# Optimization experiments

Measured on AMD Instinct MI355X. Metric: run time of the kernel, lower is better.

## Reference

```python
import jax, jax.numpy as jnp
import numpy as np

B, C, H, W = 512, 2048, 8, 8   # batch, backbone channels, feature-map HxW (cfg.output_hm_shape)
J = 30                          # smpl.pos_joint_num
CF = 512                        # conv output channels
EPS = 1e-5                      # BatchNorm eps


def setup_inputs() -> dict:
    key = jax.random.key(0)
    ks = jax.random.split(key, 10)
    D = J * (CF + 3)  # 15450
    return {
        "img_feat": jax.random.normal(ks[0], (B, C, H, W), jnp.float32),
        # joint coords in heatmap pixel space [0, W-1] (x, y, z)
        "joint_coord_img": jax.random.uniform(ks[1], (B, J, 3), jnp.float32) * (W - 1),
        "conv_w": jax.random.normal(ks[2], (CF, C), jnp.float32) * 0.02,
        "conv_b": jnp.zeros((CF,), jnp.float32),
        "bn_gamma": jnp.ones((CF,), jnp.float32),
        "bn_beta": jnp.zeros((CF,), jnp.float32),
        "bn_mean": jnp.zeros((CF,), jnp.float32),
        "bn_var": jnp.ones((CF,), jnp.float32),
        "root_w": jax.random.normal(ks[3], (6, D), jnp.float32) * 0.01,
        "root_b": jnp.zeros((6,), jnp.float32),
        "pose_w": jax.random.normal(ks[4], (126, D), jnp.float32) * 0.01,
        "pose_b": jnp.zeros((126,), jnp.float32),
        "shape_w": jax.random.normal(ks[5], (10, C), jnp.float32) * 0.01,
        "shape_b": jnp.zeros((10,), jnp.float32),
        "cam_w": jax.random.normal(ks[6], (3, C), jnp.float32) * 0.01,
        "cam_b": jnp.zeros((3,), jnp.float32),
    }


def _bilinear_sample(feat, xy):
    """Batched bilinear sample == F.grid_sample(align_corners=True, padding='zeros')
    with grid built directly from pixel coords in [0, W-1].
    feat: (B, Cf, H, W), xy: (B, J, 2) pixel coords -> (B, J, Cf)."""
    x, y = xy[..., 0], xy[..., 1]
    x0f, y0f = jnp.floor(x), jnp.floor(y)
    wx1, wy1 = x - x0f, y - y0f
    wx0, wy0 = 1.0 - wx1, 1.0 - wy1
    x0, y0 = x0f.astype(jnp.int32), y0f.astype(jnp.int32)
    x1, y1 = x0 + 1, y0 + 1

    def corner(yi, xi, wt):
        valid = (xi >= 0) & (xi < feat.shape[3]) & (yi >= 0) & (yi < feat.shape[2])
        yc = jnp.clip(yi, 0, feat.shape[2] - 1)
        xc = jnp.clip(xi, 0, feat.shape[3] - 1)
        # gather (B, Cf, J) via vmap over batch
        g = jax.vmap(lambda f, yy, xx: f[:, yy, xx])(feat, yc, xc)
        return g * (wt * valid.astype(feat.dtype))[:, None, :]

    out = (corner(y0, x0, wy0 * wx0) + corner(y0, x1, wy0 * wx1)
           + corner(y1, x0, wy1 * wx0) + corner(y1, x1, wy1 * wx1))
    return jnp.transpose(out, (0, 2, 1))  # (B, J, Cf)


def reference(img_feat, joint_coord_img, conv_w, conv_b, bn_gamma, bn_beta,
              bn_mean, bn_var, root_w, root_b, pose_w, pose_b,
              shape_w, shape_b, cam_w, cam_b):
    bsz = img_feat.shape[0]
    pooled = img_feat.mean(axis=(2, 3))                       # (B, 2048)
    shape_param = pooled @ shape_w.T + shape_b                # (B, 10)
    cam_param = pooled @ cam_w.T + cam_b                      # (B, 3)

    # 1x1 conv + BatchNorm (eval) + ReLU
    f = jnp.einsum('bchw,oc->bohw', img_feat, conv_w) + conv_b[None, :, None, None]
    f = (f - bn_mean[None, :, None, None]) * jax.lax.rsqrt(bn_var + EPS)[None, :, None, None]
    f = jax.nn.relu(f * bn_gamma[None, :, None, None] + bn_beta[None, :, None, None])

    # fused per-joint bilinear gather (replaces the per-joint python loop)
    img_feat_joints = _bilinear_sample(f, joint_coord_img[..., :2])  # (B, J, 512)
    feat = jnp.concatenate([img_feat_joints, joint_coord_img], axis=2)  # (B, J, 515)
    feat = feat.reshape(bsz, -1)                              # (B, 15450)

    root_pose = feat @ root_w.T + root_b                      # (B, 6)
    pose_param = feat @ pose_w.T + pose_b                     # (B, 126)
    return (root_pose, pose_param, shape_param, cam_param)
```

## Files before the change

kernel.cpp:

```cpp
#include <hip/hip_runtime.h>
#include <stdint.h>

typedef __attribute__((ext_vector_type(8))) short bf16x8;
typedef __attribute__((ext_vector_type(4))) float f32x4;

__device__ __forceinline__ unsigned short f2bf(float f) {
    union { float f; uint32_t u; } v; v.f = f;
    uint32_t r = (v.u + 0x7FFFu + ((v.u >> 16) & 1u)) >> 16;
    return (unsigned short)r;
}
__device__ __forceinline__ float bf2f(unsigned short u) {
    union { uint32_t u; float f; } v; v.u = ((uint32_t)u) << 16; return v.f;
}

#define WP_ELEMS  1081344
#define K2        15456
#define W2P_ELEMS (144 * K2)
#define B_OFF     42240

__global__ void pack_convw_kernel(const float* __restrict__ cw,
                                  const float* __restrict__ sw,
                                  const float* __restrict__ camw,
                                  unsigned short* __restrict__ Wp) {
    int gid = blockIdx.x * 256 + threadIdx.x;
    if (gid >= WP_ELEMS) return;
    int kt  = gid / 16896;
    int rem = gid - kt * 16896;
    int row = rem >> 5;
    int c   = rem & 31;
    int k   = kt * 32 + c;
    float v = 0.f;
    if (row < 512)      v = cw[row * 2048 + k];
    else if (row < 522) v = sw[(row - 512) * 2048 + k];
    else if (row < 525) v = camw[(row - 522) * 2048 + k];
    Wp[gid] = f2bf(v);
}

__global__ void pack_w2_kernel(const float* __restrict__ root_w,
                               const float* __restrict__ pose_w,
                               unsigned short* __restrict__ W2p) {
    int gid = blockIdx.x * 256 + threadIdx.x;
    if (gid >= W2P_ELEMS) return;
    int o2 = gid / K2;
    int kk = gid - o2 * K2;
    float v = 0.f;
    if (o2 < 132) {
        const float* wr = (o2 < 6) ? (root_w + o2 * 15450) : (pose_w + (o2 - 6) * 15450);
        if (kk < 15360) {
            int j = kk >> 9;
            int o = kk & 511;
            v = wr[j * 515 + o];
        } else {
            int c = kk - 15360;
            if (c < 90) {
                int j = c / 3, d = c - 3 * j;
                v = wr[j * 515 + 512 + d];
            }
        }
    }
    W2p[gid] = f2bf(v);
}

__global__ void bn_prep_kernel(const float* cb, const float* g, const float* be,
                               const float* m, const float* v, float* sbws) {
    int o = blockIdx.x * 256 + threadIdx.x;
    if (o >= 512) return;
    float s = g[o] * rsqrtf(v[o] + 1e-5f);
    sbws[2 * o]     = s;
    sbws[2 * o + 1] = be[o] + s * (cb[o] - m[o]);
}

__global__ __launch_bounds__(256, 2)
void conv_main_kernel(const float* __restrict__ img,
                      const float* __restrict__ jc,
                      const unsigned short* __restrict__ Wp,
                      const float* __restrict__ sbws,
                      const float* __restrict__ shape_b,
                      const float* __restrict__ cam_b,
                      unsigned short* __restrict__ sampled,
                      float* __restrict__ out) {
    __shared__ __align__(16) char smem[65536 + 256];
    const int t    = threadIdx.x;
    const int lane = t & 63;
    const int w    = t >> 6;
    const int l15  = lane & 15;
    const int quad = lane >> 4;
    const int b    = blockIdx.x;

    f32x4 acc[8][4];
    f32x4 accX;
    #pragma unroll
    for (int mi = 0; mi < 8; ++mi)
        #pragma unroll
        for (int nt = 0; nt < 4; ++nt)
            acc[mi][nt] = (f32x4){0.f, 0.f, 0.f, 0.f};
    accX = (f32x4){0.f, 0.f, 0.f, 0.f};

    const float* gBbase = img + (size_t)b * 131072 + (size_t)(w * 8) * 64 + lane;

    for (int kt = 0; kt < 64; ++kt) {
        __syncthreads();
        const int4* gA = (const int4*)(Wp + (size_t)kt * 16896);
        int4 ta[8];
        #pragma unroll
        for (int i = 0; i < 8; ++i) ta[i] = gA[t + 256 * i];
        int4 ta8;
        if (t < 64) ta8 = gA[t + 2048];
        const float* gB = gBbase + (size_t)(kt * 32) * 64;
        float fb[8];
        #pragma unroll
        for (int j = 0; j < 8; ++j) fb[j] = gB[j * 64];

        #pragma unroll
        for (int i = 0; i < 8; ++i) {
            int c2 = t + 256 * i;
            *(int4*)(smem + (c2 >> 2) * 80 + (c2 & 3) * 16) = ta[i];
        }
        if (t < 64) {
            int c2 = t + 2048;
            *(int4*)(smem + (c2 >> 2) * 80 + (c2 & 3) * 16) = ta8;
        }
        {
            int4 bv;
            bv.x = (int)((uint32_t)f2bf(fb[0]) | ((uint32_t)f2bf(fb[1]) << 16));
            bv.y = (int)((uint32_t)f2bf(fb[2]) | ((uint32_t)f2bf(fb[3]) << 16));
            bv.z = (int)((uint32_t)f2bf(fb[4]) | ((uint32_t)f2bf(fb[5]) << 16));
            bv.w = (int)((uint32_t)f2bf(fb[6]) | ((uint32_t)f2bf(fb[7]) << 16));
            *(int4*)(smem + B_OFF + lane * 80 + w * 16) = bv;
        }
        __syncthreads();

        bf16x8 bfr0 = *(const bf16x8*)(smem + B_OFF + (0  + l15) * 80 + quad * 16);
        bf16x8 bfr1 = *(const bf16x8*)(smem + B_OFF + (16 + l15) * 80 + quad * 16);
        bf16x8 bfr2 = *(const bf16x8*)(smem + B_OFF + (32 + l15) * 80 + quad * 16);
        bf16x8 bfr3 = *(const bf16x8*)(smem + B_OFF + (48 + l15) * 80 + quad * 16);
        #pragma unroll
        for (int mi = 0; mi < 8; ++mi) {
            bf16x8 afr = *(const bf16x8*)(smem + (w * 128 + mi * 16 + l15) * 80 + quad * 16);
            acc[mi][0] = __builtin_amdgcn_mfma_f32_16x16x32_bf16(afr, bfr0, acc[mi][0], 0, 0, 0);
            acc[mi][1] = __builtin_amdgcn_mfma_f32_16x16x32_bf16(afr, bfr1, acc[mi][1], 0, 0, 0);
            acc[mi][2] = __builtin_amdgcn_mfma_f32_16x16x32_bf16(afr, bfr2, acc[mi][2], 0, 0, 0);
            acc[mi][3] = __builtin_amdgcn_mfma_f32_16x16x32_bf16(afr, bfr3, acc[mi][3], 0, 0, 0);
        }
        {
            bf16x8 afrX = *(const bf16x8*)(smem + (512 + l15) * 80 + quad * 16);
            bf16x8 bfrW = *(const bf16x8*)(smem + B_OFF + (w * 16 + l15) * 80 + quad * 16);
            accX = __builtin_amdgcn_mfma_f32_16x16x32_bf16(afrX, bfrW, accX, 0, 0, 0);
        }
    }

    __syncthreads();
    const float2* sb2 = (const float2*)sbws;
    #pragma unroll
    for (int mi = 0; mi < 8; ++mi) {
        #pragma unroll
        for (int r = 0; r < 4; ++r) {
            int row = w * 128 + mi * 16 + quad * 4 + r;
            float2 sb = sb2[row];
            #pragma unroll
            for (int nt = 0; nt < 4; ++nt) {
                int col = nt * 16 + l15;
                float v = fmaxf(acc[mi][nt][r] * sb.x + sb.y, 0.f);
                *(unsigned short*)(smem + row * 128 + (((col + row) & 63) << 1)) = f2bf(v);
            }
        }
    }
    float* red = (float*)(smem + 65536);
    #pragma unroll
    for (int r = 0; r < 4; ++r) {
        float v = accX[r];
        v += __shfl_xor(v, 1);
        v += __shfl_xor(v, 2);
        v += __shfl_xor(v, 4);
        v += __shfl_xor(v, 8);
        if (l15 == 0) red[w * 16 + quad * 4 + r] = v;
    }
    __syncthreads();

    if (t < 16) {
        float v = (red[t] + red[16 + t] + red[32 + t] + red[48 + t]) * 0.015625f;
        if (t < 10)      out[67584 + b * 10 + t] = v + shape_b[t];
        else if (t < 13) out[72704 + b * 3 + (t - 10)] = v + cam_b[t - 10];
    }
    const float* jcb = jc + b * 90;
    if (t < 96) {
        float v = (t < 90) ? jcb[t] : 0.f;
        sampled[(size_t)b * K2 + 15360 + t] = f2bf(v);
    }

    unsigned int* outsamp = (unsigned int*)(sampled + (size_t)b * K2);
    const int o = 2 * t;
    for (int s = 0; s < 30; ++s) {
        float x = jcb[s * 3 + 0];
        float y = jcb[s * 3 + 1];
        float x0f = floorf(x), y0f = floorf(y);
        int x0 = (int)x0f, y0 = (int)y0f;
        int x1 = x0 + 1, y1 = y0 + 1;
        float wx1 = x - x0f, wy1 = y - y0f;
        float wx0 = 1.f - wx1, wy0 = 1.f - wy1;
        float vx0 = (x0 >= 0 && x0 < 8) ? 1.f : 0.f;
        float vx1 = (x1 >= 0 && x1 < 8) ? 1.f : 0.f;
        float vy0 = (y0 >= 0 && y0 < 8) ? 1.f : 0.f;
        float vy1 = (y1 >= 0 && y1 < 8) ? 1.f : 0.f;
        int cx0 = min(max(x0, 0), 7), cx1 = min(max(x1, 0), 7);
        int cy0 = min(max(y0, 0), 7), cy1 = min(max(y1, 0), 7);
        int p00 = cy0 * 8 + cx0, p01 = cy0 * 8 + cx1;
        int p10 = cy1 * 8 + cx0, p11 = cy1 * 8 + cx1;
        float w00 = wy0 * wx0 * vy0 * vx0, w01 = wy0 * wx1 * vy0 * vx1;
        float w10 = wy1 * wx0 * vy1 * vx0, w11 = wy1 * wx1 * vy1 * vx1;
        float vA = w00 * bf2f(*(unsigned short*)(smem + o * 128 + (((p00 + o) & 63) << 1)))
                 + w01 * bf2f(*(unsigned short*)(smem + o * 128 + (((p01 + o) & 63) << 1)))
                 + w10 * bf2f(*(unsigned short*)(smem + o * 128 + (((p10 + o) & 63) << 1)))
                 + w11 * bf2f(*(unsigned short*)(smem + o * 128 + (((p11 + o) & 63) << 1)));
        int o1 = o + 1;
        float vB = w00 * bf2f(*(unsigned short*)(smem + o1 * 128 + (((p00 + o1) & 63) << 1)))
                 + w01 * bf2f(*(unsigned short*)(smem + o1 * 128 + (((p01 + o1) & 63) << 1)))
                 + w10 * bf2f(*(unsigned short*)(smem + o1 * 128 + (((p10 + o1) & 63) << 1)))
                 + w11 * bf2f(*(unsigned short*)(smem + o1 * 128 + (((p11 + o1) & 63) << 1)));
        outsamp[s * 256 + t] = (uint32_t)f2bf(vA) | ((uint32_t)f2bf(vB) << 16);
    }
}

__global__ __launch_bounds__(256, 4)
void gemm2_kernel(const unsigned short* __restrict__ sampled,
                  const unsigned short* __restrict__ W2p,
                  float* __restrict__ part) {
    __shared__ __align__(16) char smem[16640];
    const int t    = threadIdx.x;
    const int lane = t & 63;
    const int w    = t >> 6;
    const int l15  = lane & 15;
    const int quad = lane >> 4;
    const int m0   = blockIdx.x * 64;
    const int j    = blockIdx.y;
    const int k0   = j * 512;
    const int ktn  = (j == 30) ? 3 : 16;

    f32x4 acc[9];
    #pragma unroll
    for (int nt = 0; nt < 9; ++nt) acc[nt] = (f32x4){0.f, 0.f, 0.f, 0.f};

    for (int kt = 0; kt < ktn; ++kt) {
        __syncthreads();
        {
            int r = t >> 2, ci = t & 3;
            int4 d = *(const int4*)(sampled + (size_t)(m0 + r) * K2 + k0 + kt * 32 + ci * 8);
            *(int4*)(smem + r * 80 + ci * 16) = d;
        }
        #pragma unroll
        for (int i = 0; i < 3; ++i) {
            int c2 = t + 256 * i;
            if (c2 < 576) {
                int r = c2 >> 2, ci = c2 & 3;
                int4 d = *(const int4*)(W2p + (size_t)r * K2 + k0 + kt * 32 + ci * 8);
                *(int4*)(smem + 5120 + r * 80 + ci * 16) = d;
            }
        }
        __syncthreads();
        bf16x8 a = *(const bf16x8*)(smem + (w * 16 + l15) * 80 + quad * 16);
        #pragma unroll
        for (int nt = 0; nt < 9; ++nt) {
            bf16x8 bfv = *(const bf16x8*)(smem + 5120 + (nt * 16 + l15) * 80 + quad * 16);
            acc[nt] = __builtin_amdgcn_mfma_f32_16x16x32_bf16(a, bfv, acc[nt], 0, 0, 0);
        }
    }
    float* pout = part + (size_t)(j * 8 + blockIdx.x) * 9216;
    #pragma unroll
    for (int nt = 0; nt < 9; ++nt) {
        #pragma unroll
        for (int r = 0; r < 4; ++r) {
            pout[(w * 16 + quad * 4 + r) * 144 + nt * 16 + l15] = acc[nt][r];
        }
    }
}

__global__ void reduce_out_kernel(const float* __restrict__ part,
                                  const float* __restrict__ root_b,
                                  const float* __restrict__ pose_b,
                                  float* __restrict__ out) {
    int gid = blockIdx.x * 256 + threadIdx.x;
    int m  = gid / 132;
    int o2 = gid - m * 132;
    float s = (o2 < 6) ? root_b[o2] : pose_b[o2 - 6];
    const float* p = part + (size_t)(m >> 6) * 9216 + (m & 63) * 144 + o2;
    #pragma unroll
    for (int j = 0; j < 31; ++j) s += p[(size_t)j * 8 * 9216];
    if (o2 < 6) out[m * 6 + o2] = s;
    else        out[3072 + m * 126 + (o2 - 6)] = s;
}

extern "C" void kernel_launch(void* const* d_in, const int* in_sizes, int n_in,
                              void* d_out, int out_size, void* d_ws, size_t ws_size,
                              hipStream_t stream) {
    const float* img     = (const float*)d_in[0];
    const float* jc      = (const float*)d_in[1];
    const float* conv_w  = (const float*)d_in[2];
    const float* conv_b  = (const float*)d_in[3];
    const float* bn_g    = (const float*)d_in[4];
    const float* bn_be   = (const float*)d_in[5];
    const float* bn_m    = (const float*)d_in[6];
    const float* bn_v    = (const float*)d_in[7];
    const float* root_w  = (const float*)d_in[8];
    const float* root_b  = (const float*)d_in[9];
    const float* pose_w  = (const float*)d_in[10];
    const float* pose_b  = (const float*)d_in[11];
    const float* shape_w = (const float*)d_in[12];
    const float* shape_b = (const float*)d_in[13];
    const float* cam_w   = (const float*)d_in[14];
    const float* cam_b   = (const float*)d_in[15];
    float* out = (float*)d_out;
    char* ws = (char*)d_ws;

    unsigned short* Wp   = (unsigned short*)(ws);
    unsigned short* W2p  = (unsigned short*)(ws + 2162688);
    unsigned short* samp = (unsigned short*)(ws + 6614016);
    float* part          = (float*)(ws + 22440960);
    float* sbws          = (float*)(ws + 31583232);

    pack_convw_kernel<<<4224, 256, 0, stream>>>(conv_w, shape_w, cam_w, Wp);
    pack_w2_kernel<<<8694, 256, 0, stream>>>(root_w, pose_w, W2p);
    bn_prep_kernel<<<2, 256, 0, stream>>>(conv_b, bn_g, bn_be, bn_m, bn_v, sbws);
    conv_main_kernel<<<512, 256, 0, stream>>>(img, jc, Wp, sbws, shape_b, cam_b,
                                              samp, out);
    gemm2_kernel<<<dim3(8, 31), 256, 0, stream>>>(samp, W2p, part);
    reduce_out_kernel<<<264, 256, 0, stream>>>(part, root_b, pose_b, out);
}
```

Measured before the change: 472.2 us.

## Double-buffer conv GEMM tiles with direct global-to-LDS loads for weights

```diff
diff --git a/kernel.cpp b/kernel.cpp
--- a/kernel.cpp
+++ b/kernel.cpp
@@ -13,10 +13,22 @@
     union { uint32_t u; float f; } v; v.u = ((uint32_t)u) << 16; return v.f;
 }
 
+__device__ __forceinline__ void gload16(const void* g, void* l) {
+    __builtin_amdgcn_global_load_lds(
+        (const __attribute__((address_space(1))) unsigned int*)g,
+        (__attribute__((address_space(3))) unsigned int*)l, 16, 0, 0);
+}
+
 #define WP_ELEMS  1081344
 #define K2        15456
 #define W2P_ELEMS (144 * K2)
-#define B_OFF     42240
+
+#define ABUF0  0
+#define ABUF1  33792
+#define BBUF0  67584
+#define BBUF1  71680
+#define REDOFF 75776
+#define SMEM_SZ 76032
 
 __global__ void pack_convw_kernel(const float* __restrict__ cw,
                                   const float* __restrict__ sw,
@@ -26,9 +38,13 @@
     if (gid >= WP_ELEMS) return;
     int kt  = gid / 16896;
     int rem = gid - kt * 16896;
-    int row = rem >> 5;
-    int c   = rem & 31;
-    int k   = kt * 32 + c;
+    int g   = rem >> 9;
+    int r2  = rem & 511;
+    int q   = r2 >> 7;
+    int rr  = (r2 >> 3) & 15;
+    int e   = r2 & 7;
+    int row = g * 16 + rr;
+    int k   = kt * 32 + q * 8 + e;
     float v = 0.f;
     if (row < 512)      v = cw[row * 2048 + k];
     else if (row < 522) v = sw[(row - 512) * 2048 + k];
@@ -79,7 +95,7 @@
                       const float* __restrict__ cam_b,
                       unsigned short* __restrict__ sampled,
                       float* __restrict__ out) {
-    __shared__ __align__(16) char smem[65536 + 256];
+    __shared__ __align__(16) char smem[SMEM_SZ];
     const int t    = threadIdx.x;
     const int lane = t & 63;
     const int w    = t >> 6;
@@ -97,59 +113,70 @@
     accX = (f32x4){0.f, 0.f, 0.f, 0.f};
 
     const float* gBbase = img + (size_t)b * 131072 + (size_t)(w * 8) * 64 + lane;
-
-    for (int kt = 0; kt < 64; ++kt) {
-        __syncthreads();
-        const int4* gA = (const int4*)(Wp + (size_t)kt * 16896);
-        int4 ta[8];
-        #pragma unroll
-        for (int i = 0; i < 8; ++i) ta[i] = gA[t + 256 * i];
-        int4 ta8;
-        if (t < 64) ta8 = gA[t + 2048];
+    float fb[8];
+
+    auto loadB = [&](int kt) {
         const float* gB = gBbase + (size_t)(kt * 32) * 64;
-        float fb[8];
         #pragma unroll
         for (int j = 0; j < 8; ++j) fb[j] = gB[j * 64];
-
-        #pragma unroll
-        for (int i = 0; i < 8; ++i) {
-            int c2 = t + 256 * i;
-            *(int4*)(smem + (c2 >> 2) * 80 + (c2 & 3) * 16) = ta[i];
-        }
-        if (t < 64) {
-            int c2 = t + 2048;
-            *(int4*)(smem + (c2 >> 2) * 80 + (c2 & 3) * 16) = ta8;
-        }
-        {
-            int4 bv;
-            bv.x = (int)((uint32_t)f2bf(fb[0]) | ((uint32_t)f2bf(fb[1]) << 16));
-            bv.y = (int)((uint32_t)f2bf(fb[2]) | ((uint32_t)f2bf(fb[3]) << 16));
-            bv.z = (int)((uint32_t)f2bf(fb[4]) | ((uint32_t)f2bf(fb[5]) << 16));
-            bv.w = (int)((uint32_t)f2bf(fb[6]) | ((uint32_t)f2bf(fb[7]) << 16));
-            *(int4*)(smem + B_OFF + lane * 80 + w * 16) = bv;
-        }
-        __syncthreads();
-
-        bf16x8 bfr0 = *(const bf16x8*)(smem + B_OFF + (0  + l15) * 80 + quad * 16);
-        bf16x8 bfr1 = *(const bf16x8*)(smem + B_OFF + (16 + l15) * 80 + quad * 16);
-        bf16x8 bfr2 = *(const bf16x8*)(smem + B_OFF + (32 + l15) * 80 + quad * 16);
-        bf16x8 bfr3 = *(const bf16x8*)(smem + B_OFF + (48 + l15) * 80 + quad * 16);
+    };
+    auto writeB = [&](char* bbuf) {
+        int4 bv;
+        bv.x = (int)((uint32_t)f2bf(fb[0]) | ((uint32_t)f2bf(fb[1]) << 16));
+        bv.y = (int)((uint32_t)f2bf(fb[2]) | ((uint32_t)f2bf(fb[3]) << 16));
+        bv.z = (int)((uint32_t)f2bf(fb[4]) | ((uint32_t)f2bf(fb[5]) << 16));
+        bv.w = (int)((uint32_t)f2bf(fb[6]) | ((uint32_t)f2bf(fb[7]) << 16));
+        *(int4*)(bbuf + (lane >> 4) * 1024 + w * 256 + l15 * 16) = bv;
+    };
+    auto stageA = [&](int kt, char* abuf) {
+        const unsigned short* src = Wp + (size_t)kt * 16896 + (size_t)(w * 8) * 512 + lane * 8;
+        char* dst = abuf + w * 8192;
+        #pragma unroll
+        for (int i = 0; i < 8; ++i)
+            gload16(src + i * 512, dst + i * 1024);
+        if (w == 0)
+            gload16(Wp + (size_t)kt * 16896 + 32 * 512 + lane * 8, abuf + 32768);
+    };
+    auto compute = [&](const char* abuf, const char* bbuf) {
+        bf16x8 bfr0 = *(const bf16x8*)(bbuf + 0 * 1024 + quad * 256 + l15 * 16);
+        bf16x8 bfr1 = *(const bf16x8*)(bbuf + 1 * 1024 + quad * 256 + l15 * 16);
+        bf16x8 bfr2 = *(const bf16x8*)(bbuf + 2 * 1024 + quad * 256 + l15 * 16);
+        bf16x8 bfr3 = *(const bf16x8*)(bbuf + 3 * 1024 + quad * 256 + l15 * 16);
         #pragma unroll
         for (int mi = 0; mi < 8; ++mi) {
-            bf16x8 afr = *(const bf16x8*)(smem + (w * 128 + mi * 16 + l15) * 80 + quad * 16);
+            bf16x8 afr = *(const bf16x8*)(abuf + (w * 8 + mi) * 1024 + quad * 256 + l15 * 16);
             acc[mi][0] = __builtin_amdgcn_mfma_f32_16x16x32_bf16(afr, bfr0, acc[mi][0], 0, 0, 0);
             acc[mi][1] = __builtin_amdgcn_mfma_f32_16x16x32_bf16(afr, bfr1, acc[mi][1], 0, 0, 0);
             acc[mi][2] = __builtin_amdgcn_mfma_f32_16x16x32_bf16(afr, bfr2, acc[mi][2], 0, 0, 0);
             acc[mi][3] = __builtin_amdgcn_mfma_f32_16x16x32_bf16(afr, bfr3, acc[mi][3], 0, 0, 0);
         }
         {
-            bf16x8 afrX = *(const bf16x8*)(smem + (512 + l15) * 80 + quad * 16);
-            bf16x8 bfrW = *(const bf16x8*)(smem + B_OFF + (w * 16 + l15) * 80 + quad * 16);
+            bf16x8 afrX = *(const bf16x8*)(abuf + 32768 + quad * 256 + l15 * 16);
+            bf16x8 bfrW = *(const bf16x8*)(bbuf + w * 1024 + quad * 256 + l15 * 16);
             accX = __builtin_amdgcn_mfma_f32_16x16x32_bf16(afrX, bfrW, accX, 0, 0, 0);
         }
-    }
-
+    };
+
+    loadB(0);
+    stageA(0, smem + ABUF0);
+    writeB(smem + BBUF0);
     __syncthreads();
+
+    #pragma unroll 2
+    for (int kt = 0; kt < 64; ++kt) {
+        char* acur = smem + ((kt & 1) ? ABUF1 : ABUF0);
+        char* bcur = smem + ((kt & 1) ? BBUF1 : BBUF0);
+        char* anxt = smem + ((kt & 1) ? ABUF0 : ABUF1);
+        char* bnxt = smem + ((kt & 1) ? BBUF0 : BBUF1);
+        if (kt < 63) {
+            loadB(kt + 1);
+            stageA(kt + 1, anxt);
+        }
+        compute(acur, bcur);
+        if (kt < 63) writeB(bnxt);
+        __syncthreads();
+    }
+
     const float2* sb2 = (const float2*)sbws;
     #pragma unroll
     for (int mi = 0; mi < 8; ++mi) {
@@ -165,7 +192,7 @@
             }
         }
     }
-    float* red = (float*)(smem + 65536);
+    float* red = (float*)(smem + REDOFF);
     #pragma unroll
     for (int r = 0; r < 4; ++r) {
         float v = accX[r];
```

After: 471.2 us. About the same (-0.2%).
